# Kernel optimization log

Hardware: AMD Instinct MI355X
Metric: run time of the kernel (lower is better)

Reference implementation:

```python
import jax, jax.numpy as jnp
import numpy as np

BLOCK_SIZE = 512
TOP_K = 4


def setup_inputs() -> dict:
    key = jax.random.key(0)
    k1, k2 = jax.random.split(key)
    B, H, S, D = 4, 16, 8192, 128
    q = jax.random.normal(k1, (B, H, S, D), dtype=jnp.float32)
    k = jax.random.normal(k2, (B, H, S, D), dtype=jnp.float32)
    return {"q": q, "k": k, "seq_len": S}


def reference(q, k, seq_len):
    B, H, S, D = q.shape
    num_blocks = -(-seq_len // BLOCK_SIZE)  # ceil
    pad_len = num_blocks * BLOCK_SIZE - seq_len
    if pad_len > 0:
        k = jnp.pad(k, ((0, 0), (0, 0), (0, pad_len), (0, 0)))
    # [B,H,nb,bs,D] -> mean over block -> [B,H,nb,D]
    k_mean = k.reshape(B, H, num_blocks, BLOCK_SIZE, D).mean(axis=3)
    # scores: [B,H,S,nb]
    scores = jnp.einsum('bhsd,bhnd->bhsn', q, k_mean)
    positions = jnp.arange(seq_len)
    query_block_indices = positions // BLOCK_SIZE            # [S]
    block_indices = jnp.arange(num_blocks)                   # [nb]
    causal_mask = query_block_indices[:, None] < block_indices[None, :]  # [S,nb]
    scores = jnp.where(causal_mask[None, None], -jnp.inf, scores)
    effective_top_k = min(TOP_K, num_blocks)
    _, topk_indices = jax.lax.top_k(scores, effective_top_k)  # [B,H,S,k]
    return topk_indices, query_block_indices
```

## Files before the change

### kernel.cpp

```cpp
#include <hip/hip_runtime.h>
#include <math.h>

#define BH   64
#define SEQ  8192
#define DIM  128
#define NB   16
#define BS   512

__global__ __launch_bounds__(256) void kmean_kernel(const float* __restrict__ k,
                                                    double* __restrict__ kmean_d,
                                                    int* __restrict__ qbi) {
  int gt = blockIdx.x * 256 + threadIdx.x;
  if (gt < SEQ) qbi[gt] = gt >> 9;

  int blk = blockIdx.x;
  int bh  = blk >> 4;
  int nb  = blk & 15;
  const float4* base = (const float4*)(k + ((size_t)bh * SEQ + (size_t)nb * BS) * DIM);
  int t  = threadIdx.x;
  int c4 = t & 31;
  int r0 = t >> 5;
  double a0 = 0, a1 = 0, a2 = 0, a3 = 0;
  for (int r = r0; r < BS; r += 8) {
    float4 v = base[r * 32 + c4];
    a0 += (double)v.x; a1 += (double)v.y; a2 += (double)v.z; a3 += (double)v.w;
  }
  __shared__ double red[8][32][4];
  red[r0][c4][0] = a0; red[r0][c4][1] = a1;
  red[r0][c4][2] = a2; red[r0][c4][3] = a3;
  __syncthreads();
  if (r0 == 0) {
    double s0 = 0, s1 = 0, s2 = 0, s3 = 0;
#pragma unroll
    for (int r = 0; r < 8; ++r) {
      s0 += red[r][c4][0]; s1 += red[r][c4][1];
      s2 += red[r][c4][2]; s3 += red[r][c4][3];
    }
    const double inv = 1.0 / (double)BS;
    double2* dst = (double2*)kmean_d + ((size_t)(bh * NB + nb) * 32 + c4) * 2;
    double2 o0, o1;
    o0.x = s0 * inv; o0.y = s1 * inv;
    o1.x = s2 * inv; o1.y = s3 * inv;
    dst[0] = o0; dst[1] = o1;
  }
}

__global__ __launch_bounds__(256) void score_topk_kernel(const float* __restrict__ q,
                                                         const double* __restrict__ kmean_d,
                                                         int* __restrict__ out) {
  __shared__ double2 kkd[NB * 64];
  __shared__ float4  qs[4][256];

  int t      = threadIdx.x;
  int qstart = blockIdx.x * 256;
  int bh     = qstart >> 13;

  const double2* ksrc = (const double2*)kmean_d + (size_t)bh * NB * 64;
#pragma unroll
  for (int i = 0; i < 4; ++i) kkd[i * 256 + t] = ksrc[i * 256 + t];
  __syncthreads();

  int wave = t >> 6;
  int lane = t & 63;
  int qw   = qstart + wave * 64;
  int qb   = (qw & (SEQ - 1)) >> 9;
  int qbs  = __builtin_amdgcn_readfirstlane(qb);

  int fc = lane & 3;
  int rr = lane >> 2;

  const float4* qbase = (const float4*)(q + (size_t)qw * DIM);
  float4* myqs = qs[wave];

  double ps[NB];
#pragma unroll
  for (int n = 0; n < NB; ++n) ps[n] = 0.0;

  float4 ld[4];
#pragma unroll
  for (int i = 0; i < 4; ++i)
    ld[i] = qbase[(size_t)(i * 16 + rr) * 32 + fc];

  for (int c = 0; c < 8; ++c) {
#pragma unroll
    for (int i = 0; i < 4; ++i)
      myqs[(i * 16 + rr) * 4 + (fc ^ (rr & 3))] = ld[i];
    __builtin_amdgcn_wave_barrier();

    double qd[16];
#pragma unroll
    for (int j = 0; j < 4; ++j) {
      float4 v = myqs[lane * 4 + (j ^ (lane & 3))];
      qd[4 * j + 0] = (double)v.x; qd[4 * j + 1] = (double)v.y;
      qd[4 * j + 2] = (double)v.z; qd[4 * j + 3] = (double)v.w;
    }

    if (c < 7) {
#pragma unroll
      for (int i = 0; i < 4; ++i)
        ld[i] = qbase[(size_t)(i * 16 + rr) * 32 + (c + 1) * 4 + fc];
    }

#pragma unroll
    for (int n = 0; n < NB; ++n) {
      if (n <= qbs) {
        const double2* kr = &kkd[n * 64 + c * 8];
        double a = ps[n];
#pragma unroll
        for (int j2 = 0; j2 < 8; ++j2) {
          double2 kv = kr[j2];
          a = fma(qd[2 * j2],     kv.x, a);
          a = fma(qd[2 * j2 + 1], kv.y, a);
        }
        ps[n] = a;
      }
    }
  }

  unsigned long long keys[NB];
#pragma unroll
  for (int n = 0; n < NB; ++n) {
    double v = (n <= qbs) ? ps[n] : -INFINITY;
    long long u = __double_as_longlong(v);
    unsigned long long sk =
        (unsigned long long)(u ^ ((u >> 63) | 0x8000000000000000LL));
    keys[n] = (sk & ~0xFULL) | (unsigned long long)(15 - n);
  }
  int res[4];
#pragma unroll
  for (int pp = 0; pp < 4; ++pp) {
    unsigned long long best = keys[0];
#pragma unroll
    for (int n = 1; n < NB; ++n) best = (keys[n] > best) ? keys[n] : best;
    res[pp] = 15 - (int)(best & 0xFULL);
#pragma unroll
    for (int n = 0; n < NB; ++n) keys[n] = (keys[n] == best) ? 0ULL : keys[n];
  }

  int myq = qw + lane;
  *(int4*)(out + (size_t)myq * 4) = make_int4(res[0], res[1], res[2], res[3]);
}

extern "C" void kernel_launch(void* const* d_in, const int* in_sizes, int n_in,
                              void* d_out, int out_size, void* d_ws, size_t ws_size,
                              hipStream_t stream) {
  (void)in_sizes; (void)n_in; (void)out_size; (void)ws_size;
  const float* q = (const float*)d_in[0];
  const float* k = (const float*)d_in[1];
  double* kmean_d = (double*)d_ws;
  int*    out     = (int*)d_out;
  int*    qbi     = out + (size_t)BH * SEQ * 4;

  hipLaunchKernelGGL(kmean_kernel, dim3(BH * NB), dim3(256), 0, stream,
                     k, kmean_d, qbi);
  hipLaunchKernelGGL(score_topk_kernel, dim3(BH * SEQ / 256), dim3(256), 0, stream,
                     q, kmean_d, out);
}
```

Measured before the change: 591.8 us.

## Process two queries per thread and read block means from global memory

Each thread now accumulates scores for two query rows, so every key-mean value it loads feeds two FMAs, and each block covers 512 queries instead of 256. The shared-memory staging of the double-precision block means is removed; those values are read straight from global memory at addresses that are the same across the wave, relying on cache or scalar loads. Staging of the q tile is reorganised into 16 chunks of 8 dimensions, with an extra wave barrier per chunk. The trade is twice as many live double accumulators (higher register pressure, lower occupancy) and half as many blocks launched.

```diff
diff --git a/kernel.cpp b/kernel.cpp
--- a/kernel.cpp
+++ b/kernel.cpp
@@ -45,100 +45,100 @@
   }
 }
 
+
+#define TOPK_STORE(PS, QIDX)                                                   \
+  {                                                                            \
+    unsigned long long keys[NB];                                               \
+_Pragma("unroll")                                                              \
+    for (int n = 0; n < NB; ++n) {                                             \
+      double v = (n <= qbs) ? PS[n] : -INFINITY;                               \
+      long long u = __double_as_longlong(v);                                   \
+      unsigned long long sk =                                                  \
+          (unsigned long long)(u ^ ((u >> 63) | 0x8000000000000000LL));        \
+      keys[n] = (sk & ~0xFULL) | (unsigned long long)(15 - n);                 \
+    }                                                                          \
+    int res[4];                                                                \
+_Pragma("unroll")                                                              \
+    for (int pp = 0; pp < 4; ++pp) {                                           \
+      unsigned long long best = keys[0];                                       \
+_Pragma("unroll")                                                              \
+      for (int n = 1; n < NB; ++n) best = (keys[n] > best) ? keys[n] : best;   \
+      res[pp] = 15 - (int)(best & 0xFULL);                                     \
+_Pragma("unroll")                                                              \
+      for (int n = 0; n < NB; ++n) keys[n] = (keys[n] == best) ? 0ULL : keys[n];\
+    }                                                                          \
+    *(int4*)(out + (size_t)(QIDX) * 4) = make_int4(res[0], res[1], res[2], res[3]); \
+  }
+
 __global__ __launch_bounds__(256) void score_topk_kernel(const float* __restrict__ q,
                                                          const double* __restrict__ kmean_d,
                                                          int* __restrict__ out) {
-  __shared__ double2 kkd[NB * 64];
-  __shared__ float4  qs[4][256];
+  __shared__ float4 qs[4][256];
 
   int t      = threadIdx.x;
-  int qstart = blockIdx.x * 256;
+  int qstart = blockIdx.x * 512;
   int bh     = qstart >> 13;
+  int wave   = t >> 6;
+  int lane   = t & 63;
+  int qw     = qstart + wave * 128;
+  int qbs    = __builtin_amdgcn_readfirstlane((qw & (SEQ - 1)) >> 9);
 
-  const double2* ksrc = (const double2*)kmean_d + (size_t)bh * NB * 64;
-#pragma unroll
-  for (int i = 0; i < 4; ++i) kkd[i * 256 + t] = ksrc[i * 256 + t];
-  __syncthreads();
-
-  int wave = t >> 6;
-  int lane = t & 63;
-  int qw   = qstart + wave * 64;
-  int qb   = (qw & (SEQ - 1)) >> 9;
-  int qbs  = __builtin_amdgcn_readfirstlane(qb);
-
-  int fc = lane & 3;
-  int rr = lane >> 2;
-
+  const double* kbh   = kmean_d + (size_t)bh * NB * DIM;
   const float4* qbase = (const float4*)(q + (size_t)qw * DIM);
   float4* myqs = qs[wave];
 
-  double ps[NB];
+  int srow = lane >> 1;
+  int sf   = lane & 1;
+
+  double ps0[NB], ps1[NB];
 #pragma unroll
-  for (int n = 0; n < NB; ++n) ps[n] = 0.0;
+  for (int n = 0; n < NB; ++n) { ps0[n] = 0.0; ps1[n] = 0.0; }
 
   float4 ld[4];
 #pragma unroll
   for (int i = 0; i < 4; ++i)
-    ld[i] = qbase[(size_t)(i * 16 + rr) * 32 + fc];
+    ld[i] = qbase[(size_t)(i * 32 + srow) * 32 + sf];
 
-  for (int c = 0; c < 8; ++c) {
+  for (int c = 0; c < 16; ++c) {
 #pragma unroll
-    for (int i = 0; i < 4; ++i)
-      myqs[(i * 16 + rr) * 4 + (fc ^ (rr & 3))] = ld[i];
+    for (int i = 0; i < 4; ++i) myqs[i * 64 + lane] = ld[i];
     __builtin_amdgcn_wave_barrier();
 
-    double qd[16];
-#pragma unroll
-    for (int j = 0; j < 4; ++j) {
-      float4 v = myqs[lane * 4 + (j ^ (lane & 3))];
-      qd[4 * j + 0] = (double)v.x; qd[4 * j + 1] = (double)v.y;
-      qd[4 * j + 2] = (double)v.z; qd[4 * j + 3] = (double)v.w;
-    }
+    float4 a0 = myqs[2 * lane];
+    float4 a1 = myqs[2 * lane + 1];
+    float4 b0 = myqs[2 * (lane + 64)];
+    float4 b1 = myqs[2 * (lane + 64) + 1];
+    double qa[8], qb[8];
+    qa[0] = (double)a0.x; qa[1] = (double)a0.y; qa[2] = (double)a0.z; qa[3] = (double)a0.w;
+    qa[4] = (double)a1.x; qa[5] = (double)a1.y; qa[6] = (double)a1.z; qa[7] = (double)a1.w;
+    qb[0] = (double)b0.x; qb[1] = (double)b0.y; qb[2] = (double)b0.z; qb[3] = (double)b0.w;
+    qb[4] = (double)b1.x; qb[5] = (double)b1.y; qb[6] = (double)b1.z; qb[7] = (double)b1.w;
 
-    if (c < 7) {
+    if (c < 15) {
 #pragma unroll
       for (int i = 0; i < 4; ++i)
-        ld[i] = qbase[(size_t)(i * 16 + rr) * 32 + (c + 1) * 4 + fc];
+        ld[i] = qbase[(size_t)(i * 32 + srow) * 32 + (c + 1) * 2 + sf];
     }
 
 #pragma unroll
     for (int n = 0; n < NB; ++n) {
       if (n <= qbs) {
-        const double2* kr = &kkd[n * 64 + c * 8];
-        double a = ps[n];
+        const double* kr = kbh + n * DIM + c * 8;
+        double x0 = ps0[n], x1 = ps1[n];
 #pragma unroll
-        for (int j2 = 0; j2 < 8; ++j2) {
-          double2 kv = kr[j2];
-          a = fma(qd[2 * j2],     kv.x, a);
-          a = fma(qd[2 * j2 + 1], kv.y, a);
+        for (int j = 0; j < 8; ++j) {
+          double kv = kr[j];
+          x0 = fma(qa[j], kv, x0);
+          x1 = fma(qb[j], kv, x1);
         }
-        ps[n] = a;
+        ps0[n] = x0; ps1[n] = x1;
       }
     }
+    __builtin_amdgcn_wave_barrier();
   }
 
-  unsigned long long keys[NB];
-#pragma unroll
-  for (int n = 0; n < NB; ++n) {
-    double v = (n <= qbs) ? ps[n] : -INFINITY;
-    long long u = __double_as_longlong(v);
-    unsigned long long sk =
-        (unsigned long long)(u ^ ((u >> 63) | 0x8000000000000000LL));
-    keys[n] = (sk & ~0xFULL) | (unsigned long long)(15 - n);
-  }
-  int res[4];
-#pragma unroll
-  for (int pp = 0; pp < 4; ++pp) {
-    unsigned long long best = keys[0];
-#pragma unroll
-    for (int n = 1; n < NB; ++n) best = (keys[n] > best) ? keys[n] : best;
-    res[pp] = 15 - (int)(best & 0xFULL);
-#pragma unroll
-    for (int n = 0; n < NB; ++n) keys[n] = (keys[n] == best) ? 0ULL : keys[n];
-  }
-
-  int myq = qw + lane;
-  *(int4*)(out + (size_t)myq * 4) = make_int4(res[0], res[1], res[2], res[3]);
+  TOPK_STORE(ps0, qw + lane);
+  TOPK_STORE(ps1, qw + 64 + lane);
 }
 
 extern "C" void kernel_launch(void* const* d_in, const int* in_sizes, int n_in,
@@ -153,6 +153,6 @@
 
   hipLaunchKernelGGL(kmean_kernel, dim3(BH * NB), dim3(256), 0, stream,
                      k, kmean_d, qbi);
-  hipLaunchKernelGGL(score_topk_kernel, dim3(BH * SEQ / 256), dim3(256), 0, stream,
+  hipLaunchKernelGGL(score_topk_kernel, dim3(BH * SEQ / 512), dim3(256), 0, stream,
                      q, kmean_d, out);
 }
```

Measured after the change: 697.0 us. 1.18x slower.

## Read k-means directly from global memory as uniform loads, pad q staging

Applied to the files above, without the earlier changes.

The block no longer stages the double-precision block means into LDS behind a block barrier. Each wave now reads them straight from global memory at wave-uniform addresses, which the compiler can turn into scalar loads. The q staging buffer changes from an XOR swizzle to row padding (stride 20 floats), and a second wave barrier is added at the end of each chunk. This removes the LDS fill, the __syncthreads and the per-element LDS reads of the key means, at the cost of depending on scalar cache hits and possibly more global load latency.

```diff
diff --git a/kernel.cpp b/kernel.cpp
--- a/kernel.cpp
+++ b/kernel.cpp
@@ -45,82 +45,78 @@
   }
 }
 
+
+#define ACC(N, P)                                                              \
+  if (qbs >= (N)) {                                                            \
+    const double* kr_##P = kbh + (N) * DIM + c * 16;                           \
+    _Pragma("unroll")                                                          \
+    for (int j = 0; j < 16; ++j) P = fma(qd[j], kr_##P[j], P);                 \
+  }
+
 __global__ __launch_bounds__(256) void score_topk_kernel(const float* __restrict__ q,
                                                          const double* __restrict__ kmean_d,
                                                          int* __restrict__ out) {
-  __shared__ double2 kkd[NB * 64];
-  __shared__ float4  qs[4][256];
+  __shared__ float qs[4][64 * 20];
 
   int t      = threadIdx.x;
   int qstart = blockIdx.x * 256;
   int bh     = qstart >> 13;
+  int wave   = t >> 6;
+  int lane   = t & 63;
+  int qw     = qstart + wave * 64;
+  int qbs    = __builtin_amdgcn_readfirstlane((qw & (SEQ - 1)) >> 9);
 
-  const double2* ksrc = (const double2*)kmean_d + (size_t)bh * NB * 64;
-#pragma unroll
-  for (int i = 0; i < 4; ++i) kkd[i * 256 + t] = ksrc[i * 256 + t];
-  __syncthreads();
+  const double* kbh   = kmean_d + (size_t)bh * NB * DIM;
+  const float4* qbase = (const float4*)(q + (size_t)qw * DIM);
+  float* myqs = qs[wave];
 
-  int wave = t >> 6;
-  int lane = t & 63;
-  int qw   = qstart + wave * 64;
-  int qb   = (qw & (SEQ - 1)) >> 9;
-  int qbs  = __builtin_amdgcn_readfirstlane(qb);
+  int sr = lane >> 2;
+  int sc = lane & 3;
 
-  int fc = lane & 3;
-  int rr = lane >> 2;
-
-  const float4* qbase = (const float4*)(q + (size_t)qw * DIM);
-  float4* myqs = qs[wave];
-
-  double ps[NB];
-#pragma unroll
-  for (int n = 0; n < NB; ++n) ps[n] = 0.0;
+  double p0 = 0, p1 = 0, p2 = 0, p3 = 0, p4 = 0, p5 = 0, p6 = 0, p7 = 0;
+  double p8 = 0, p9 = 0, p10 = 0, p11 = 0, p12 = 0, p13 = 0, p14 = 0, p15 = 0;
 
   float4 ld[4];
 #pragma unroll
   for (int i = 0; i < 4; ++i)
-    ld[i] = qbase[(size_t)(i * 16 + rr) * 32 + fc];
+    ld[i] = qbase[(size_t)(i * 16 + sr) * 32 + sc];
 
   for (int c = 0; c < 8; ++c) {
 #pragma unroll
     for (int i = 0; i < 4; ++i)
-      myqs[(i * 16 + rr) * 4 + (fc ^ (rr & 3))] = ld[i];
+      *(float4*)&myqs[(i * 16 + sr) * 20 + 4 * sc] = ld[i];
     __builtin_amdgcn_wave_barrier();
 
+    float4 f0 = *(const float4*)&myqs[lane * 20 + 0];
+    float4 f1 = *(const float4*)&myqs[lane * 20 + 4];
+    float4 f2 = *(const float4*)&myqs[lane * 20 + 8];
+    float4 f3 = *(const float4*)&myqs[lane * 20 + 12];
     double qd[16];
-#pragma unroll
-    for (int j = 0; j < 4; ++j) {
-      float4 v = myqs[lane * 4 + (j ^ (lane & 3))];
-      qd[4 * j + 0] = (double)v.x; qd[4 * j + 1] = (double)v.y;
-      qd[4 * j + 2] = (double)v.z; qd[4 * j + 3] = (double)v.w;
-    }
+    qd[0]  = (double)f0.x; qd[1]  = (double)f0.y; qd[2]  = (double)f0.z; qd[3]  = (double)f0.w;
+    qd[4]  = (double)f1.x; qd[5]  = (double)f1.y; qd[6]  = (double)f1.z; qd[7]  = (double)f1.w;
+    qd[8]  = (double)f2.x; qd[9]  = (double)f2.y; qd[10] = (double)f2.z; qd[11] = (double)f2.w;
+    qd[12] = (double)f3.x; qd[13] = (double)f3.y; qd[14] = (double)f3.z; qd[15] = (double)f3.w;
 
     if (c < 7) {
 #pragma unroll
       for (int i = 0; i < 4; ++i)
-        ld[i] = qbase[(size_t)(i * 16 + rr) * 32 + (c + 1) * 4 + fc];
+        ld[i] = qbase[(size_t)(i * 16 + sr) * 32 + 4 * (c + 1) + sc];
     }
 
-#pragma unroll
-    for (int n = 0; n < NB; ++n) {
-      if (n <= qbs) {
-        const double2* kr = &kkd[n * 64 + c * 8];
-        double a = ps[n];
-#pragma unroll
-        for (int j2 = 0; j2 < 8; ++j2) {
-          double2 kv = kr[j2];
-          a = fma(qd[2 * j2],     kv.x, a);
-          a = fma(qd[2 * j2 + 1], kv.y, a);
-        }
-        ps[n] = a;
-      }
-    }
+    ACC(0,  p0)  ACC(1,  p1)  ACC(2,  p2)  ACC(3,  p3)
+    ACC(4,  p4)  ACC(5,  p5)  ACC(6,  p6)  ACC(7,  p7)
+    ACC(8,  p8)  ACC(9,  p9)  ACC(10, p10) ACC(11, p11)
+    ACC(12, p12) ACC(13, p13) ACC(14, p14) ACC(15, p15)
+
+    __builtin_amdgcn_wave_barrier();
   }
 
+  double psv[NB] = {p0, p1, p2,  p3,  p4,  p5,  p6,  p7,
+                    p8, p9, p10, p11, p12, p13, p14, p15};
   unsigned long long keys[NB];
 #pragma unroll
   for (int n = 0; n < NB; ++n) {
-    double v = (n <= qbs) ? ps[n] : -INFINITY;
+    double v = (n <= qbs) ? psv[n] : -INFINITY;
     long long u = __double_as_longlong(v);
     unsigned long long sk =
         (unsigned long long)(u ^ ((u >> 63) | 0x8000000000000000LL));
@@ -136,9 +132,7 @@
 #pragma unroll
     for (int n = 0; n < NB; ++n) keys[n] = (keys[n] == best) ? 0ULL : keys[n];
   }
-
-  int myq = qw + lane;
-  *(int4*)(out + (size_t)myq * 4) = make_int4(res[0], res[1], res[2], res[3]);
+  *(int4*)(out + (size_t)(qw + lane) * 4) = make_int4(res[0], res[1], res[2], res[3]);
 }
 
 extern "C" void kernel_launch(void* const* d_in, const int* in_sizes, int n_in,
```

Result: slower. 608.7 us (+2.9%).
